# Kernel optimization log

Hardware: AMD Instinct MI355X
Metric: run time of the kernel (lower is better)

## Reference

```python
import jax, jax.numpy as jnp
import numpy as np

H, D = 8, 16          # heads, per-head dim (hidden_channels=128)
HID = H * D
N = 200000            # movie nodes
E = 500000            # edges per metapath relation
IN = 256              # input feature dim
CLS = 3               # output classes


def setup_inputs() -> dict:
    key = jax.random.key(0)
    ks = jax.random.split(key, 13)
    return {
        "x_movie": jax.random.normal(ks[0], (N, IN), jnp.float32),
        "W_proj": jax.random.normal(ks[1], (IN, HID), jnp.float32) * 0.05,
        "b_proj": jnp.zeros((HID,), jnp.float32),
        "att_src0": jax.random.normal(ks[2], (H, D), jnp.float32) * 0.1,
        "att_dst0": jax.random.normal(ks[3], (H, D), jnp.float32) * 0.1,
        "att_src1": jax.random.normal(ks[4], (H, D), jnp.float32) * 0.1,
        "att_dst1": jax.random.normal(ks[5], (H, D), jnp.float32) * 0.1,
        "q": jax.random.normal(ks[6], (HID,), jnp.float32) * 0.1,
        "k_w": jax.random.normal(ks[7], (HID, HID), jnp.float32) * 0.05,
        "k_b": jnp.zeros((HID,), jnp.float32),
        "lin_w": jax.random.normal(ks[8], (HID, CLS), jnp.float32) * 0.05,
        "lin_b": jnp.zeros((CLS,), jnp.float32),
        "e0_src": jax.random.randint(ks[9], (E,), 0, N, jnp.int32),
        "e0_dst": jax.random.randint(ks[10], (E,), 0, N, jnp.int32),
        "e1_src": jax.random.randint(ks[11], (E,), 0, N, jnp.int32),
        "e1_dst": jax.random.randint(ks[12], (E,), 0, N, jnp.int32),
    }


def _han_rel(h, att_s, att_d, src, dst, n):
    # h: [N, H, D]; GAT-style per-relation attention with segment softmax over dst
    a_s = jnp.sum(h * att_s, axis=-1)                      # [N, H]
    a_d = jnp.sum(h * att_d, axis=-1)                      # [N, H]
    alpha = jax.nn.leaky_relu(a_s[src] + a_d[dst], 0.2)    # [E, H]
    m = jax.ops.segment_max(alpha, dst, num_segments=n)    # per-dst max
    ex = jnp.exp(alpha - m[dst])
    den = jax.ops.segment_sum(ex, dst, num_segments=n)
    w = ex / (den[dst] + 1e-16)                            # edge softmax (PyG eps)
    msg = (h[src] * w[:, :, None]).reshape(-1, HID)        # [E, HID]
    return jax.nn.relu(jax.ops.segment_sum(msg, dst, num_segments=n))


def reference(x_movie, W_proj, b_proj, att_src0, att_dst0, att_src1, att_dst1,
              q, k_w, k_b, lin_w, lin_b, e0_src, e0_dst, e1_src, e1_dst):
    # node-type projection (HANConv.proj), dropout omitted (eval mode)
    h = (x_movie @ W_proj + b_proj).reshape(-1, H, D)      # [N, H, D]
    out0 = _han_rel(h, att_src0, att_dst0, e0_src, e0_dst, N)  # [N, HID]
    out1 = _han_rel(h, att_src1, att_dst1, e1_src, e1_dst, N)
    # semantic-level attention (HANConv.group)
    outs = jnp.stack([out0, out1])                         # [M=2, N, HID]
    score = jnp.sum(jnp.tanh(outs @ k_w + k_b).mean(axis=1) * q, axis=-1)  # [M]
    beta = jax.nn.softmax(score)
    fused = jnp.einsum('m,mnf->nf', beta, outs)            # [N, HID]
    return fused @ lin_w + lin_b                           # [N, CLS]
```

## Files before the change

kernel.cpp:

```cpp
#include <hip/hip_runtime.h>


typedef __attribute__((ext_vector_type(8))) short bf16x8;
typedef __attribute__((ext_vector_type(4))) float f32x4;
typedef __attribute__((ext_vector_type(8))) unsigned short ushort8;

__device__ __forceinline__ unsigned short f2b(float f) {
  union { float f; unsigned u; } v; v.f = f;
  unsigned r = v.u + 0x7fffu + ((v.u >> 16) & 1u);
  return (unsigned short)(r >> 16);
}
__device__ __forceinline__ float b2f(unsigned short u) {
  union { unsigned u; float f; } v; v.u = ((unsigned)u) << 16;
  return v.f;
}
__device__ __forceinline__ float fast_tanh(float x) {
  x = fminf(fmaxf(x, -15.f), 15.f);
  float t = __expf(2.f * x);
  return 1.f - 2.f / (t + 1.f);
}
__device__ __forceinline__ void gload_lds16(const void* g, void* l) {
  __builtin_amdgcn_global_load_lds(
      (const __attribute__((address_space(1))) unsigned int*)g,
      (__attribute__((address_space(3))) unsigned int*)l, 16, 0, 0);
}

__global__ __launch_bounds__(256) void prep_lite(
    const int* __restrict__ e0d, const int* __restrict__ e1d,
    int* __restrict__ deg, int ne, int n,
    const float* __restrict__ Wp, const float* __restrict__ kwm,
    unsigned short* __restrict__ Wpf, unsigned short* __restrict__ Kwf) {
  const int tid = threadIdx.x;
  int b = blockIdx.x;
  const int cb = (2 * ne + 255) >> 8;
  if (b < cb) {
    int e = b * 256 + tid;
    if (e < ne) atomicAdd(&deg[e0d[e]], 1);
    else if (e < 2 * ne) atomicAdd(&deg[n + e1d[e - ne]], 1);
    return;
  }
  b -= cb;
  int t = b * 256 + tid;
  const float* W; unsigned short* Wf; int idx;
  if (t < 4096) { W = Wp; Wf = Wpf; idx = t; }
  else if (t < 6144) { W = kwm; Wf = Kwf; idx = t - 4096; }
  else return;
  int lane = idx & 63, nt = (idx >> 6) & 7, kt = idx >> 9;
  int c = lane & 15, ks = lane >> 4;
  int kbase = kt * 32 + ks * 8;
  int col = nt * 16 + c;
  ushort8 o;
#pragma unroll
  for (int j = 0; j < 8; ++j) o[j] = f2b(W[(size_t)(kbase + j) * 128 + col]);
  *(ushort8*)(Wf + (size_t)idx * 8) = o;
}

__global__ __launch_bounds__(256) void proj_mfma(
    const float* __restrict__ X, const unsigned short* __restrict__ Wf,
    const float* __restrict__ bias,
    const float* __restrict__ as0v, const float* __restrict__ ad0v,
    const float* __restrict__ as1v, const float* __restrict__ ad1v,
    unsigned short* __restrict__ Hb, float* __restrict__ preb, int n) {
  __shared__ float atsf[16384];
  const int tid = threadIdx.x;
  const int wid = tid >> 6, lane = tid & 63;
  const int wm = wid >> 1, wn = wid & 1;
  const int row0 = blockIdx.x * 64;
  const int r = lane & 15, ks = lane >> 4;

  {
    float* dstbase = atsf + wid * 16 * 256;
#pragma unroll
    for (int i = 0; i < 16; ++i) {
      int row = wid * 16 + i;
      int grow = row0 + row;
      grow = grow < n ? grow : n - 1;
      const float* src = X + (size_t)grow * 256 + ((lane ^ (i & 7)) * 4);
      gload_lds16(src, dstbase + i * 256);
    }
  }
  __syncthreads();

  f32x4 acc[2][4] = {};
  const unsigned short* bptr = Wf + ((size_t)(wn * 4) * 64 + lane) * 8;
  const int sw = r & 7;
#pragma unroll
  for (int kt = 0; kt < 8; ++kt) {
    const int c0 = kt * 8 + ks * 2;
    bf16x8 a[2], b[4];
#pragma unroll
    for (int mi = 0; mi < 2; ++mi) {
      const float* lrow = atsf + (wm * 32 + mi * 16 + r) * 256;
      float4 f0 = *(const float4*)(lrow + ((c0 ^ sw) * 4));
      float4 f1 = *(const float4*)(lrow + (((c0 + 1) ^ sw) * 4));
      bf16x8 v;
      v[0] = (short)f2b(f0.x); v[1] = (short)f2b(f0.y);
      v[2] = (short)f2b(f0.z); v[3] = (short)f2b(f0.w);
      v[4] = (short)f2b(f1.x); v[5] = (short)f2b(f1.y);
      v[6] = (short)f2b(f1.z); v[7] = (short)f2b(f1.w);
      a[mi] = v;
    }
#pragma unroll
    for (int ni = 0; ni < 4; ++ni)
      b[ni] = *(const bf16x8*)(bptr + ((size_t)kt * 8 + ni) * 512);
#pragma unroll
    for (int mi = 0; mi < 2; ++mi)
#pragma unroll
      for (int ni = 0; ni < 4; ++ni)
        acc[mi][ni] = __builtin_amdgcn_mfma_f32_16x16x32_bf16(a[mi], b[ni], acc[mi][ni], 0, 0, 0);
  }
  __syncthreads();

  unsigned short* ct = (unsigned short*)atsf;
#pragma unroll
  for (int ni = 0; ni < 4; ++ni) {
    const int col = wn * 64 + ni * 16 + r;
    const float bv = bias[col];
#pragma unroll
    for (int mi = 0; mi < 2; ++mi)
#pragma unroll
      for (int i = 0; i < 4; ++i)
        ct[(wm * 32 + mi * 16 + ks * 4 + i) * 136 + col] = f2b(acc[mi][ni][i] + bv);
  }
  __syncthreads();

  {
    int row = tid >> 2, qq = tid & 3;
    int grow = row0 + row;
    if (grow < n) {
      ushort8* dst = (ushort8*)(Hb + (size_t)grow * 128 + qq * 32);
#pragma unroll
      for (int j = 0; j < 4; ++j) dst[j] = *(ushort8*)&ct[row * 136 + qq * 32 + j * 8];
    }
  }

  const size_t n8 = (size_t)n * 8;
  for (int rh = tid; rh < 512; rh += 256) {
    int row = rh >> 3, head = rh & 7;
    int node = row0 + row;
    if (node < n) {
      float hv[16];
#pragma unroll
      for (int j = 0; j < 16; ++j) hv[j] = b2f(ct[row * 136 + head * 16 + j]);
      float s0 = 0, d0 = 0, s1 = 0, d1 = 0;
      const float* p0 = as0v + head * 16;
      const float* p1 = ad0v + head * 16;
      const float* p2 = as1v + head * 16;
      const float* p3 = ad1v + head * 16;
#pragma unroll
      for (int j = 0; j < 16; ++j) {
        float v = hv[j];
        s0 += v * p0[j]; d0 += v * p1[j];
        s1 += v * p2[j]; d1 += v * p3[j];
      }
      size_t idx = (size_t)node * 8 + head;
      preb[idx] = s0;
      preb[n8 + idx] = d0;
      preb[2 * n8 + idx] = s1;
      preb[3 * n8 + idx] = d1;
    }
  }
}

__global__ __launch_bounds__(256) void scan1_kernel(
    const int* __restrict__ deg, int* __restrict__ pre, int* __restrict__ bsum, int m) {
  __shared__ int sd[256];
  int t = threadIdx.x;
  int base = blockIdx.x * 2048 + t * 8;
  int v[8], sum = 0;
#pragma unroll
  for (int j = 0; j < 8; ++j) {
    v[j] = (base + j < m) ? deg[base + j] : 0;
    sum += v[j];
  }
  sd[t] = sum;
  __syncthreads();
  for (int off = 1; off < 256; off <<= 1) {
    int x = (t >= off) ? sd[t - off] : 0;
    __syncthreads();
    if (t >= off) sd[t] += x;
    __syncthreads();
  }
  if (t == 255) bsum[blockIdx.x] = sd[255];
  int run = sd[t] - sum;
#pragma unroll
  for (int j = 0; j < 8; ++j) {
    if (base + j < m) pre[base + j] = run;
    run += v[j];
  }
}

__global__ __launch_bounds__(256) void scan2_kernel(int* __restrict__ bsum, int nb) {
  __shared__ int sd[256];
  int t = threadIdx.x;
  int v = (t < nb) ? bsum[t] : 0;
  sd[t] = v;
  __syncthreads();
  for (int off = 1; off < 256; off <<= 1) {
    int x = (t >= off) ? sd[t - off] : 0;
    __syncthreads();
    if (t >= off) sd[t] += x;
    __syncthreads();
  }
  if (t < nb) bsum[t] = sd[t] - v;
}

__global__ void scan3_kernel(int* __restrict__ pre, const int* __restrict__ bsum, int m, int total) {
  int i = blockIdx.x * 256 + threadIdx.x;
  if (i < m) pre[i] += bsum[i >> 11];
  if (i == m) pre[m] = total;
}

__global__ void fill2_kernel(const int* __restrict__ e0s, const int* __restrict__ e0d,
                             const int* __restrict__ e1s, const int* __restrict__ e1d,
                             const int* __restrict__ pre, int* __restrict__ cur,
                             int* __restrict__ csr, int ne, int n) {
  int e = blockIdx.x * 256 + threadIdx.x;
  int s, idx;
  if (e < ne) { idx = e0d[e]; s = e0s[e]; }
  else if (e < 2 * ne) { idx = n + e1d[e - ne]; s = e1s[e - ne]; }
  else return;
  int slot = pre[idx] + atomicAdd(&cur[idx], 1);
  csr[slot] = s;
}

__global__ __launch_bounds__(256) void agg2_kernel(
    const int* __restrict__ pre, const int* __restrict__ csr,
    const unsigned short* __restrict__ Hb, const float* __restrict__ preb,
    unsigned short* __restrict__ outb, int n) {
  int rel = blockIdx.y;
  int gid = blockIdx.x * 256 + threadIdx.x;
  int node = gid >> 3;
  int lane = gid & 7;
  if (node >= n) return;
  const size_t n8 = (size_t)n * 8;
  const float* a_s = preb + (size_t)(2 * rel) * n8;
  const float* a_d = preb + (size_t)(2 * rel + 1) * n8;
  int beg = pre[rel * n + node], end = pre[rel * n + node + 1];
  float ad = a_d[(size_t)node * 8 + lane];
  float s = 0.f;
  float acc[16] = {};
  int e = beg;
  for (; e + 1 < end; e += 2) {
    int s0 = csr[e], s1 = csr[e + 1];
    float al0 = a_s[(size_t)s0 * 8 + lane] + ad;
    float al1 = a_s[(size_t)s1 * 8 + lane] + ad;
    const ushort8* h0p = (const ushort8*)(Hb + (size_t)s0 * 128 + lane * 16);
    const ushort8* h1p = (const ushort8*)(Hb + (size_t)s1 * 128 + lane * 16);
    ushort8 h0a = h0p[0], h0b = h0p[1];
    ushort8 h1a = h1p[0], h1b = h1p[1];
    al0 = (al0 >= 0.f) ? al0 : 0.2f * al0;
    al1 = (al1 >= 0.f) ? al1 : 0.2f * al1;
    float p0 = __expf(al0), p1 = __expf(al1);
    s += p0 + p1;
#pragma unroll
    for (int j = 0; j < 8; ++j) {
      acc[j]     += p0 * b2f(h0a[j]) + p1 * b2f(h1a[j]);
      acc[8 + j] += p0 * b2f(h0b[j]) + p1 * b2f(h1b[j]);
    }
  }
  if (e < end) {
    int s0 = csr[e];
    float al0 = a_s[(size_t)s0 * 8 + lane] + ad;
    const ushort8* h0p = (const ushort8*)(Hb + (size_t)s0 * 128 + lane * 16);
    ushort8 h0a = h0p[0], h0b = h0p[1];
    al0 = (al0 >= 0.f) ? al0 : 0.2f * al0;
    float p0 = __expf(al0);
    s += p0;
#pragma unroll
    for (int j = 0; j < 8; ++j) {
      acc[j]     += p0 * b2f(h0a[j]);
      acc[8 + j] += p0 * b2f(h0b[j]);
    }
  }
  float inv = 1.f / (s + 1e-16f);
  ushort8 o0, o1;
#pragma unroll
  for (int j = 0; j < 8; ++j) {
    o0[j] = f2b(fmaxf(acc[j] * inv, 0.f));
    o1[j] = f2b(fmaxf(acc[8 + j] * inv, 0.f));
  }
  ushort8* dst = (ushort8*)(outb + (size_t)rel * n * 128 + (size_t)node * 128 + lane * 16);
  dst[0] = o0;
  dst[1] = o1;
}

__global__ __launch_bounds__(256) void score2_mfma(
    const unsigned short* __restrict__ outb, const unsigned short* __restrict__ Kf,
    const float* __restrict__ kb, const float* __restrict__ q,
    const float* __restrict__ lw, float* __restrict__ pout,
    float* __restrict__ sb, int n) {
  __shared__ unsigned short at[16384];
  __shared__ float red[256];
  const int rel = blockIdx.y;
  const unsigned short* A = outb + (size_t)rel * n * 128;
  const int tid = threadIdx.x;
  const int wid = tid >> 6, lane = tid & 63;
  const int wm = wid >> 1, wn = wid & 1;
  const int row0 = blockIdx.x * 128;
  const int r = lane & 15, ks = lane >> 4;

  {
    unsigned short* dstbase = at + wid * 4096;
#pragma unroll
    for (int i = 0; i < 8; ++i) {
      int chunk = i * 64 + lane;
      int row = wid * 32 + (chunk >> 4);
      int c = chunk & 15;
      int grow = row0 + row;
      grow = grow < n ? grow : n - 1;
      const unsigned short* src = A + (size_t)grow * 128 + ((c ^ (row & 7)) * 8);
      gload_lds16(src, dstbase + i * 512);
    }
  }
  __syncthreads();

  f32x4 acc[4][4] = {};
  const unsigned short* bptr = Kf + ((size_t)(wn * 4) * 64 + lane) * 8;
#pragma unroll
  for (int kt = 0; kt < 4; ++kt) {
    bf16x8 a[4], b[4];
#pragma unroll
    for (int mi = 0; mi < 4; ++mi) {
      int row = wm * 64 + mi * 16 + r;
      a[mi] = *(const bf16x8*)&at[row * 128 + (((kt * 4 + ks) ^ (row & 7)) * 8)];
    }
#pragma unroll
    for (int ni = 0; ni < 4; ++ni)
      b[ni] = *(const bf16x8*)(bptr + ((size_t)kt * 8 + ni) * 512);
#pragma unroll
    for (int mi = 0; mi < 4; ++mi)
#pragma unroll
      for (int ni = 0; ni < 4; ++ni)
        acc[mi][ni] = __builtin_amdgcn_mfma_f32_16x16x32_bf16(a[mi], b[ni], acc[mi][ni], 0, 0, 0);
  }

  if (tid < 128) {
    int node = row0 + tid;
    if (node < n) {
      float p0 = 0.f, p1 = 0.f, p2 = 0.f;
      int s = tid & 7;
#pragma unroll
      for (int c = 0; c < 16; ++c) {
        const unsigned short* rp = &at[tid * 128 + ((c ^ s) * 8)];
#pragma unroll
        for (int j = 0; j < 8; ++j) {
          float v = b2f(rp[j]);
          const float* w = lw + (size_t)(c * 8 + j) * 3;
          p0 += v * w[0]; p1 += v * w[1]; p2 += v * w[2];
        }
      }
      float4 o = make_float4(p0, p1, p2, 0.f);
      *(float4*)(pout + (size_t)node * 8 + rel * 4) = o;
    }
  }

  float part = 0.f;
#pragma unroll
  for (int ni = 0; ni < 4; ++ni) {
    const int col = wn * 64 + ni * 16 + r;
    const float kbv = kb[col], qv = q[col];
#pragma unroll
    for (int mi = 0; mi < 4; ++mi) {
#pragma unroll
      for (int i = 0; i < 4; ++i) {
        int row = row0 + wm * 64 + mi * 16 + ks * 4 + i;
        if (row < n) part += fast_tanh(acc[mi][ni][i] + kbv) * qv;
      }
    }
  }
  red[tid] = part;
  __syncthreads();
  for (int off = 128; off > 0; off >>= 1) {
    if (tid < off) red[tid] += red[tid + off];
    __syncthreads();
  }
  if (tid == 0) atomicAdd(&sb[rel], red[0]);
}

__global__ void beta_kernel(float* __restrict__ sb, float invn) {
  if (threadIdx.x == 0 && blockIdx.x == 0) {
    float s0 = sb[0] * invn, s1 = sb[1] * invn;
    float m = fmaxf(s0, s1);
    float e0 = __expf(s0 - m), e1 = __expf(s1 - m);
    float d = e0 + e1;
    sb[2] = e0 / d;
    sb[3] = e1 / d;
  }
}

__global__ __launch_bounds__(256) void final2_kernel(
    const float* __restrict__ pout, const float* __restrict__ sb,
    const float* __restrict__ lb, float* __restrict__ out, int n) {
  int node = blockIdx.x * 256 + threadIdx.x;
  if (node >= n) return;
  float b0 = sb[2], b1 = sb[3];
  const float4* p = (const float4*)(pout + (size_t)node * 8);
  float4 pa = p[0], pb = p[1];
  float* d = out + (size_t)node * 3;
  d[0] = b0 * pa.x + b1 * pb.x + lb[0];
  d[1] = b0 * pa.y + b1 * pb.y + lb[1];
  d[2] = b0 * pa.z + b1 * pb.z + lb[2];
}

extern "C" void kernel_launch(void* const* d_in, const int* in_sizes, int n_in,
                              void* d_out, int out_size, void* d_ws, size_t ws_size,
                              hipStream_t stream) {
  const float* x   = (const float*)d_in[0];
  const float* Wp  = (const float*)d_in[1];
  const float* bp  = (const float*)d_in[2];
  const float* as0 = (const float*)d_in[3];
  const float* ad0 = (const float*)d_in[4];
  const float* as1 = (const float*)d_in[5];
  const float* ad1 = (const float*)d_in[6];
  const float* q   = (const float*)d_in[7];
  const float* kw  = (const float*)d_in[8];
  const float* kb  = (const float*)d_in[9];
  const float* lw  = (const float*)d_in[10];
  const float* lb  = (const float*)d_in[11];
  const int* e0s = (const int*)d_in[12];
  const int* e0d = (const int*)d_in[13];
  const int* e1s = (const int*)d_in[14];
  const int* e1d = (const int*)d_in[15];
  const int n  = in_sizes[0] / 256;
  const int ne = in_sizes[12];
  float* out = (float*)d_out;

  char* ws = (char*)d_ws;
  size_t off = 0;
  auto alloc = [&](size_t b) -> char* {
    char* p = ws + off;
    off = (off + b + 255) & ~(size_t)255;
    return p;
  };
  unsigned short* h    = (unsigned short*)alloc((size_t)n * 128 * 2);
  unsigned short* outb = (unsigned short*)alloc((size_t)2 * n * 128 * 2);
  float* preb = (float*)alloc((size_t)4 * n * 8 * 4);
  float* pout = (float*)alloc((size_t)n * 8 * 4);
  int* pre    = (int*)alloc((size_t)(2 * n + 1) * 4);
  int* csr    = (int*)alloc((size_t)2 * ne * 4);
  int* deg    = (int*)alloc(((size_t)4 * n + 4) * 4);
  int* cur    = deg + 2 * n;
  float* sb   = (float*)(deg + 4 * n);
  int* bsum   = (int*)alloc(256 * 4);
  unsigned short* Wpf = (unsigned short*)alloc((size_t)4096 * 8 * 2);
  unsigned short* Kwf = (unsigned short*)alloc((size_t)2048 * 8 * 2);

  const int m = 2 * n;
  const int nblk_scan = (m + 2047) / 2048;
  const int cnt_blks = (2 * ne + 255) / 256;

  hipMemsetAsync(deg, 0, ((size_t)4 * n + 4) * 4, stream);
  hipLaunchKernelGGL(prep_lite, dim3(cnt_blks + 24), dim3(256), 0, stream,
                     e0d, e1d, deg, ne, n, Wp, kw, Wpf, Kwf);

  const int gproj = (n + 63) / 64;
  hipLaunchKernelGGL(proj_mfma, dim3(gproj), dim3(256), 0, stream,
                     x, Wpf, bp, as0, ad0, as1, ad1, h, preb, n);

  hipLaunchKernelGGL(scan1_kernel, dim3(nblk_scan), dim3(256), 0, stream, deg, pre, bsum, m);
  hipLaunchKernelGGL(scan2_kernel, dim3(1), dim3(256), 0, stream, bsum, nblk_scan);
  hipLaunchKernelGGL(scan3_kernel, dim3((m + 1 + 255) / 256), dim3(256), 0, stream,
                     pre, bsum, m, 2 * ne);
  hipLaunchKernelGGL(fill2_kernel, dim3((2 * ne + 255) / 256), dim3(256), 0, stream,
                     e0s, e0d, e1s, e1d, pre, cur, csr, ne, n);
  hipLaunchKernelGGL(agg2_kernel, dim3((n * 8 + 255) / 256, 2), dim3(256), 0, stream,
                     pre, csr, h, preb, outb, n);

  hipLaunchKernelGGL(score2_mfma, dim3((n + 127) / 128, 2), dim3(256), 0, stream,
                     outb, Kwf, kb, q, lw, pout, sb, n);
  hipLaunchKernelGGL(beta_kernel, dim3(1), dim3(64), 0, stream, sb, 1.0f / n);
  hipLaunchKernelGGL(final2_kernel, dim3((n + 255) / 256), dim3(256), 0, stream,
                     pout, sb, lb, out, n);
}
```

Baseline: 350.5 us.

## Double-buffer K-chunks of X in projection GEMM to overlap loads with MFMA

```diff
diff --git a/kernel.cpp b/kernel.cpp
--- a/kernel.cpp
+++ b/kernel.cpp
@@ -61,57 +61,72 @@
     const float* __restrict__ as0v, const float* __restrict__ ad0v,
     const float* __restrict__ as1v, const float* __restrict__ ad1v,
     unsigned short* __restrict__ Hb, float* __restrict__ preb, int n) {
-  __shared__ float atsf[16384];
+  __shared__ float buf[2][4096];
   const int tid = threadIdx.x;
   const int wid = tid >> 6, lane = tid & 63;
   const int wm = wid >> 1, wn = wid & 1;
   const int row0 = blockIdx.x * 64;
   const int r = lane & 15, ks = lane >> 4;
 
-  {
-    float* dstbase = atsf + wid * 16 * 256;
-#pragma unroll
-    for (int i = 0; i < 16; ++i) {
-      int row = wid * 16 + i;
-      int grow = row0 + row;
-      grow = grow < n ? grow : n - 1;
-      const float* src = X + (size_t)grow * 256 + ((lane ^ (i & 7)) * 4);
-      gload_lds16(src, dstbase + i * 256);
-    }
-  }
-  __syncthreads();
-
   f32x4 acc[2][4] = {};
   const unsigned short* bptr = Wf + ((size_t)(wn * 4) * 64 + lane) * 8;
-  const int sw = r & 7;
-#pragma unroll
-  for (int kt = 0; kt < 8; ++kt) {
-    const int c0 = kt * 8 + ks * 2;
-    bf16x8 a[2], b[4];
-#pragma unroll
-    for (int mi = 0; mi < 2; ++mi) {
-      const float* lrow = atsf + (wm * 32 + mi * 16 + r) * 256;
-      float4 f0 = *(const float4*)(lrow + ((c0 ^ sw) * 4));
-      float4 f1 = *(const float4*)(lrow + (((c0 + 1) ^ sw) * 4));
-      bf16x8 v;
-      v[0] = (short)f2b(f0.x); v[1] = (short)f2b(f0.y);
-      v[2] = (short)f2b(f0.z); v[3] = (short)f2b(f0.w);
-      v[4] = (short)f2b(f1.x); v[5] = (short)f2b(f1.y);
-      v[6] = (short)f2b(f1.z); v[7] = (short)f2b(f1.w);
-      a[mi] = v;
-    }
-#pragma unroll
-    for (int ni = 0; ni < 4; ++ni)
-      b[ni] = *(const bf16x8*)(bptr + ((size_t)kt * 8 + ni) * 512);
-#pragma unroll
-    for (int mi = 0; mi < 2; ++mi)
-#pragma unroll
-      for (int ni = 0; ni < 4; ++ni)
-        acc[mi][ni] = __builtin_amdgcn_mfma_f32_16x16x32_bf16(a[mi], b[ni], acc[mi][ni], 0, 0, 0);
-  }
-  __syncthreads();
-
-  unsigned short* ct = (unsigned short*)atsf;
+
+#define STAGE(b, s)                                                            \
+  {                                                                            \
+    _Pragma("unroll")                                                          \
+    for (int i = 0; i < 4; ++i) {                                              \
+      int rloc = wid * 16 + i * 4 + ks;                                        \
+      int grow = row0 + rloc;                                                  \
+      grow = grow < n ? grow : n - 1;                                          \
+      const float* src =                                                       \
+          X + (size_t)grow * 256 + (s) * 64 + ((r ^ (rloc & 7)) << 2);         \
+      gload_lds16(src, &buf[b][(wid * 16 + i * 4) * 64]);                      \
+    }                                                                          \
+  }
+
+#define COMPUTE(b, s)                                                          \
+  {                                                                            \
+    _Pragma("unroll")                                                          \
+    for (int kt = 0; kt < 2; ++kt) {                                           \
+      bf16x8 a[2], bb[4];                                                      \
+      _Pragma("unroll")                                                        \
+      for (int mi = 0; mi < 2; ++mi) {                                         \
+        int rr = wm * 32 + mi * 16 + r;                                        \
+        const float* lrow = &buf[b][rr * 64];                                  \
+        int c0 = kt * 8 + ks * 2;                                              \
+        int sw = rr & 7;                                                       \
+        float4 f0 = *(const float4*)(lrow + ((c0 ^ sw) * 4));                  \
+        float4 f1 = *(const float4*)(lrow + (((c0 + 1) ^ sw) * 4));            \
+        bf16x8 v;                                                              \
+        v[0] = (short)f2b(f0.x); v[1] = (short)f2b(f0.y);                      \
+        v[2] = (short)f2b(f0.z); v[3] = (short)f2b(f0.w);                      \
+        v[4] = (short)f2b(f1.x); v[5] = (short)f2b(f1.y);                      \
+        v[6] = (short)f2b(f1.z); v[7] = (short)f2b(f1.w);                      \
+        a[mi] = v;                                                             \
+      }                                                                        \
+      _Pragma("unroll")                                                        \
+      for (int ni = 0; ni < 4; ++ni)                                           \
+        bb[ni] = *(const bf16x8*)(bptr + (((size_t)(s) * 2 + kt) * 8 + ni) * 512); \
+      _Pragma("unroll")                                                        \
+      for (int mi = 0; mi < 2; ++mi)                                           \
+        _Pragma("unroll")                                                      \
+        for (int ni = 0; ni < 4; ++ni)                                         \
+          acc[mi][ni] = __builtin_amdgcn_mfma_f32_16x16x32_bf16(               \
+              a[mi], bb[ni], acc[mi][ni], 0, 0, 0);                            \
+    }                                                                          \
+  }
+
+  STAGE(0, 0);
+  __syncthreads();
+  STAGE(1, 1); COMPUTE(0, 0); __syncthreads();
+  STAGE(0, 2); COMPUTE(1, 1); __syncthreads();
+  STAGE(1, 3); COMPUTE(0, 2); __syncthreads();
+  COMPUTE(1, 3);
+  __syncthreads();
+#undef STAGE
+#undef COMPUTE
+
+  unsigned short* ct = (unsigned short*)&buf[0][0];
 #pragma unroll
   for (int ni = 0; ni < 4; ++ni) {
     const int col = wn * 64 + ni * 16 + r;
```

New measurement: 335.8 us. 4.2% less time.

## Pipeline projection GEMM with register double-buffering and 128-row tiles per block

Applied to the files above, without the earlier changes.

```diff
diff --git a/kernel.cpp b/kernel.cpp
--- a/kernel.cpp
+++ b/kernel.cpp
@@ -61,81 +61,106 @@
     const float* __restrict__ as0v, const float* __restrict__ ad0v,
     const float* __restrict__ as1v, const float* __restrict__ ad1v,
     unsigned short* __restrict__ Hb, float* __restrict__ preb, int n) {
-  __shared__ float atsf[16384];
+  __shared__ unsigned short lds[17408];
   const int tid = threadIdx.x;
   const int wid = tid >> 6, lane = tid & 63;
-  const int wm = wid >> 1, wn = wid & 1;
-  const int row0 = blockIdx.x * 64;
+  const int row0 = blockIdx.x * 128;
+  const int wrow0 = row0 + wid * 32;
   const int r = lane & 15, ks = lane >> 4;
+  const int r2 = lane >> 1, ch = lane & 1;
+
+  unsigned short* abuf = lds + wid * 1280;
+  int growL = wrow0 + r2; growL = growL < n ? growL : n - 1;
+  const float4* f4row = (const float4*)(X + (size_t)growL * 256 + ch * 16);
+  const unsigned short* WfL = Wf + lane * 8;
+
+  f32x4 acc[2][8] = {};
+
+#define LOADSTAGE(P, s) { const float4* fp = f4row + (s) * 8;                  \
+    P[0] = fp[0]; P[1] = fp[1]; P[2] = fp[2]; P[3] = fp[3]; }
+
+#define WRITESTAGE(P) { ushort8 o0, o1;                                        \
+    o0[0] = f2b(P[0].x); o0[1] = f2b(P[0].y); o0[2] = f2b(P[0].z);             \
+    o0[3] = f2b(P[0].w); o0[4] = f2b(P[1].x); o0[5] = f2b(P[1].y);             \
+    o0[6] = f2b(P[1].z); o0[7] = f2b(P[1].w);                                  \
+    o1[0] = f2b(P[2].x); o1[1] = f2b(P[2].y); o1[2] = f2b(P[2].z);             \
+    o1[3] = f2b(P[2].w); o1[4] = f2b(P[3].x); o1[5] = f2b(P[3].y);             \
+    o1[6] = f2b(P[3].z); o1[7] = f2b(P[3].w);                                  \
+    *(ushort8*)&abuf[r2 * 40 + ch * 16] = o0;                                  \
+    *(ushort8*)&abuf[r2 * 40 + ch * 16 + 8] = o1; }
+
+#define BBLOAD(P, s) { _Pragma("unroll")                                       \
+    for (int ni = 0; ni < 8; ++ni)                                             \
+      P[ni] = *(const bf16x8*)(WfL + ((size_t)(s) * 8 + ni) * 512); }
+
+#define COMPUTE(P) { bf16x8 aV0, aV1;                                          \
+    aV0 = *(const bf16x8*)&abuf[r * 40 + ks * 8];                              \
+    aV1 = *(const bf16x8*)&abuf[(16 + r) * 40 + ks * 8];                       \
+    _Pragma("unroll")                                                          \
+    for (int ni = 0; ni < 8; ++ni) {                                           \
+      acc[0][ni] = __builtin_amdgcn_mfma_f32_16x16x32_bf16(aV0, P[ni], acc[0][ni], 0, 0, 0); \
+      acc[1][ni] = __builtin_amdgcn_mfma_f32_16x16x32_bf16(aV1, P[ni], acc[1][ni], 0, 0, 0); \
+    } }
+
+#define STEP(s, CA, CB, NB, WN)                                                \
+  asm volatile("s_waitcnt vmcnt(" WN ")" ::: "memory");                        \
+  __builtin_amdgcn_sched_barrier(0);                                           \
+  WRITESTAGE(CA);                                                              \
+  if ((s) < 7) BBLOAD(NB, (s) + 1);                                            \
+  if ((s) < 6) LOADSTAGE(CA, (s) + 2);                                         \
+  asm volatile("s_waitcnt lgkmcnt(0)" ::: "memory");                           \
+  __builtin_amdgcn_sched_barrier(0);                                           \
+  COMPUTE(CB);
+
+  float4 A0[4], A1[4];
+  bf16x8 B0[8], B1[8];
+
+  LOADSTAGE(A0, 0);
+  BBLOAD(B0, 0);
+  LOADSTAGE(A1, 1);
+
+  STEP(0, A0, B0, B1, "12")
+  STEP(1, A1, B1, B0, "12")
+  STEP(2, A0, B0, B1, "12")
+  STEP(3, A1, B1, B0, "12")
+  STEP(4, A0, B0, B1, "12")
+  STEP(5, A1, B1, B0, "12")
+  STEP(6, A0, B0, B1, "12")
+  STEP(7, A1, B1, B0, "8")
+
+#undef LOADSTAGE
+#undef WRITESTAGE
+#undef BBLOAD
+#undef COMPUTE
+#undef STEP
+
+  __syncthreads();
+
+  unsigned short* ct = lds;
+#pragma unroll
+  for (int ni = 0; ni < 8; ++ni) {
+    const int col = ni * 16 + r;
+    const float bv = bias[col];
+#pragma unroll
+    for (int mi = 0; mi < 2; ++mi)
+#pragma unroll
+      for (int i = 0; i < 4; ++i)
+        ct[(wid * 32 + mi * 16 + ks * 4 + i) * 136 + col] = f2b(acc[mi][ni][i] + bv);
+  }
+  __syncthreads();
 
   {
-    float* dstbase = atsf + wid * 16 * 256;
-#pragma unroll
-    for (int i = 0; i < 16; ++i) {
-      int row = wid * 16 + i;
-      int grow = row0 + row;
-      grow = grow < n ? grow : n - 1;
-      const float* src = X + (size_t)grow * 256 + ((lane ^ (i & 7)) * 4);
-      gload_lds16(src, dstbase + i * 256);
-    }
-  }
-  __syncthreads();
-
-  f32x4 acc[2][4] = {};
-  const unsigned short* bptr = Wf + ((size_t)(wn * 4) * 64 + lane) * 8;
-  const int sw = r & 7;
-#pragma unroll
-  for (int kt = 0; kt < 8; ++kt) {
-    const int c0 = kt * 8 + ks * 2;
-    bf16x8 a[2], b[4];
-#pragma unroll
-    for (int mi = 0; mi < 2; ++mi) {
-      const float* lrow = atsf + (wm * 32 + mi * 16 + r) * 256;
-      float4 f0 = *(const float4*)(lrow + ((c0 ^ sw) * 4));
-      float4 f1 = *(const float4*)(lrow + (((c0 + 1) ^ sw) * 4));
-      bf16x8 v;
-      v[0] = (short)f2b(f0.x); v[1] = (short)f2b(f0.y);
-      v[2] = (short)f2b(f0.z); v[3] = (short)f2b(f0.w);
-      v[4] = (short)f2b(f1.x); v[5] = (short)f2b(f1.y);
-      v[6] = (short)f2b(f1.z); v[7] = (short)f2b(f1.w);
-      a[mi] = v;
-    }
-#pragma unroll
-    for (int ni = 0; ni < 4; ++ni)
-      b[ni] = *(const bf16x8*)(bptr + ((size_t)kt * 8 + ni) * 512);
-#pragma unroll
-    for (int mi = 0; mi < 2; ++mi)
-#pragma unroll
-      for (int ni = 0; ni < 4; ++ni)
-        acc[mi][ni] = __builtin_amdgcn_mfma_f32_16x16x32_bf16(a[mi], b[ni], acc[mi][ni], 0, 0, 0);
-  }
-  __syncthreads();
-
-  unsigned short* ct = (unsigned short*)atsf;
-#pragma unroll
-  for (int ni = 0; ni < 4; ++ni) {
-    const int col = wn * 64 + ni * 16 + r;
-    const float bv = bias[col];
-#pragma unroll
-    for (int mi = 0; mi < 2; ++mi)
-#pragma unroll
-      for (int i = 0; i < 4; ++i)
-        ct[(wm * 32 + mi * 16 + ks * 4 + i) * 136 + col] = f2b(acc[mi][ni][i] + bv);
-  }
-  __syncthreads();
-
-  {
-    int row = tid >> 2, qq = tid & 3;
+    int row = tid >> 1, half = tid & 1;
     int grow = row0 + row;
     if (grow < n) {
-      ushort8* dst = (ushort8*)(Hb + (size_t)grow * 128 + qq * 32);
-#pragma unroll
-      for (int j = 0; j < 4; ++j) dst[j] = *(ushort8*)&ct[row * 136 + qq * 32 + j * 8];
+      ushort8* dst = (ushort8*)(Hb + (size_t)grow * 128 + half * 64);
+#pragma unroll
+      for (int j = 0; j < 8; ++j) dst[j] = *(ushort8*)&ct[row * 136 + half * 64 + j * 8];
     }
   }
 
   const size_t n8 = (size_t)n * 8;
-  for (int rh = tid; rh < 512; rh += 256) {
+  for (int rh = tid; rh < 1024; rh += 256) {
     int row = rh >> 3, head = rh & 7;
     int node = row0 + row;
     if (node < n) {
@@ -454,7 +479,7 @@
   hipLaunchKernelGGL(prep_lite, dim3(cnt_blks + 24), dim3(256), 0, stream,
                      e0d, e1d, deg, ne, n, Wp, kw, Wpf, Kwf);
 
-  const int gproj = (n + 63) / 64;
+  const int gproj = (n + 127) / 128;
   hipLaunchKernelGGL(proj_mfma, dim3(gproj), dim3(256), 0, stream,
                      x, Wpf, bp, as0, ad0, as1, ad1, h, preb, n);
 
```

Result: faster. 340.3 us (-2.9%).
